# Optimization experiments

Hardware: AMD Instinct MI355X
Metric: run time of the kernel (lower is better)

## Reference

```python
import jax, jax.numpy as jnp
import numpy as np

B, C, H, W = 4, 512, 64, 64
NUM_GROUPS = 32
EPS = 1e-6


def setup_inputs() -> dict:
    key = jax.random.key(0)
    ks = jax.random.split(key, 5)
    s = 1.0 / np.sqrt(C)
    return {
        "x": jax.random.normal(ks[0], (B, C, H, W), dtype=jnp.float32),
        "gn_scale": jnp.ones((C,), jnp.float32),
        "gn_bias": jnp.zeros((C,), jnp.float32),
        "wq": jax.random.normal(ks[1], (C, C), jnp.float32) * s,
        "bq": jnp.zeros((C,), jnp.float32),
        "wk": jax.random.normal(ks[2], (C, C), jnp.float32) * s,
        "bk": jnp.zeros((C,), jnp.float32),
        "wv": jax.random.normal(ks[3], (C, C), jnp.float32) * s,
        "bv": jnp.zeros((C,), jnp.float32),
        "wo": jax.random.normal(ks[4], (C, C), jnp.float32) * s,
        "bo": jnp.zeros((C,), jnp.float32),
    }


def _group_norm(x, scale, bias):
    # x: [b, c, h, w]; normalize over (c//g, h, w) within each of g groups
    b, c, h, w = x.shape
    g = NUM_GROUPS
    xg = x.reshape(b, g, c // g, h, w)
    mean = jnp.mean(xg, axis=(2, 3, 4), keepdims=True)
    var = jnp.var(xg, axis=(2, 3, 4), keepdims=True)
    xg = (xg - mean) * jax.lax.rsqrt(var + EPS)
    xn = xg.reshape(b, c, h, w)
    return xn * scale[None, :, None, None] + bias[None, :, None, None]


def _conv1x1(x, w, b):
    # channel-mixing 1x1 conv: [b, c, h, w] x [c_in, c_out] -> [b, c_out, h, w]
    return jnp.einsum('bchw,cd->bdhw', x, w) + b[None, :, None, None]


def reference(x, gn_scale, gn_bias, wq, bq, wk, bk, wv, bv, wo, bo):
    b, c, h, w = x.shape
    h_ = _group_norm(x, gn_scale, gn_bias)
    q = _conv1x1(h_, wq, bq).reshape(b, c, h * w).transpose(0, 2, 1)  # [b, hw, c]
    k = _conv1x1(h_, wk, bk).reshape(b, c, h * w)                     # [b, c, hw]
    v = _conv1x1(h_, wv, bv).reshape(b, c, h * w)                     # [b, c, hw]
    scores = jnp.matmul(q, k) * (c ** -0.5)      # [b, hw, hw]
    attn = jax.nn.softmax(scores, axis=-1)       # [b, hw, hw]
    out = jnp.matmul(v, attn.transpose(0, 2, 1)) # [b, c, hw]
    out = out.reshape(b, c, h, w)
    out = _conv1x1(out, wo, bo)
    return x + out
```

## Files before the change

### kernel.cpp

```cpp
#include <hip/hip_runtime.h>
#include <stdint.h>

typedef __attribute__((ext_vector_type(8))) short short8;
typedef __attribute__((ext_vector_type(4))) float f32x4;
typedef __attribute__((ext_vector_type(16))) float f32x16;
typedef __attribute__((ext_vector_type(4))) unsigned int uint4v;

__device__ __forceinline__ short cvt_bf16(float f) {
  uint32_t u = __builtin_bit_cast(uint32_t, f);
  u += 0x7FFFu + ((u >> 16) & 1u);
  return (short)(u >> 16);
}

__device__ __forceinline__ float bf16_to_f32(short s) {
  return __builtin_bit_cast(float, (uint32_t)((unsigned short)s) << 16);
}

__device__ __forceinline__ void gload_lds16(const void* g, void* l) {
  __builtin_amdgcn_global_load_lds(
      (const __attribute__((address_space(1))) void*)g,
      (__attribute__((address_space(3))) void*)l, 16, 0, 0);
}

__global__ __launch_bounds__(256) void k_transpose_w(const float* __restrict__ src,
                                                     short* __restrict__ dst) {
  __shared__ float t[32][33];
  int n0 = blockIdx.x * 32, c0 = blockIdx.y * 32;
  int lx = threadIdx.x & 31, ly = threadIdx.x >> 5;
#pragma unroll
  for (int i = 0; i < 4; ++i) {
    int c = ly + i * 8;
    t[c][lx] = src[(size_t)(c0 + c) * 512 + n0 + lx];
  }
  __syncthreads();
#pragma unroll
  for (int i = 0; i < 4; ++i) {
    int n = ly + i * 8;
    dst[(size_t)(n0 + n) * 512 + c0 + lx] = cvt_bf16(t[lx][n]);
  }
}

__global__ void k_bias_concat(const float* __restrict__ bq, const float* __restrict__ bk,
                              float* __restrict__ bqk) {
  int i = blockIdx.x * 256 + threadIdx.x;
  if (i < 512) bqk[i] = bq[i];
  else if (i < 1024) bqk[i] = bk[i - 512];
}

__global__ __launch_bounds__(256) void k_gn_stats(const float* __restrict__ x,
                                                  float* __restrict__ stats) {
  int bg = blockIdx.x;
  const float* p = x + (size_t)bg * 65536;
  float s = 0.f, ss = 0.f;
#pragma unroll 4
  for (int i = 0; i < 64; ++i) {
    float4 v = *(const float4*)(p + i * 1024 + threadIdx.x * 4);
    s += v.x + v.y + v.z + v.w;
    ss += v.x * v.x + v.y * v.y + v.z * v.z + v.w * v.w;
  }
#pragma unroll
  for (int m = 1; m < 64; m <<= 1) {
    s += __shfl_xor(s, m, 64);
    ss += __shfl_xor(ss, m, 64);
  }
  __shared__ float red[8];
  int w = threadIdx.x >> 6;
  if ((threadIdx.x & 63) == 0) { red[w * 2] = s; red[w * 2 + 1] = ss; }
  __syncthreads();
  if (threadIdx.x == 0) {
    float S1 = red[0] + red[2] + red[4] + red[6];
    float S2 = red[1] + red[3] + red[5] + red[7];
    float mean = S1 * (1.f / 65536.f);
    float var = S2 * (1.f / 65536.f) - mean * mean;
    stats[bg * 2] = mean;
    stats[bg * 2 + 1] = rsqrtf(var + 1e-6f);
  }
}

__global__ __launch_bounds__(256) void k_gn_apply(const float* __restrict__ x,
    const float* __restrict__ stats, const float* __restrict__ gsc,
    const float* __restrict__ gbi, short* __restrict__ h_t) {
  __shared__ float t[64][65];
  int p0 = blockIdx.x * 64, c0 = blockIdx.y * 64, b = blockIdx.z;
  int lp = threadIdx.x & 63, lc = threadIdx.x >> 6;
#pragma unroll
  for (int i = 0; i < 16; ++i) {
    int c = c0 + lc * 16 + i;
    float mean = stats[(b * 32 + (c >> 4)) * 2];
    float rstd = stats[(b * 32 + (c >> 4)) * 2 + 1];
    float v = x[((size_t)b * 512 + c) * 4096 + p0 + lp];
    t[lc * 16 + i][lp] = (v - mean) * rstd * gsc[c] + gbi[c];
  }
  __syncthreads();
  int pl = threadIdx.x >> 2;
  int cs = (threadIdx.x & 3) * 16;
  short8 v8a, v8b;
#pragma unroll
  for (int j = 0; j < 8; ++j) v8a[j] = cvt_bf16(t[cs + j][pl]);
#pragma unroll
  for (int j = 0; j < 8; ++j) v8b[j] = cvt_bf16(t[cs + 8 + j][pl]);
  size_t o = ((size_t)(b * 4096 + p0 + pl)) * 512 + c0 + cs;
  *(short8*)(h_t + o) = v8a;
  *(short8*)(h_t + o + 8) = v8b;
}

template <int BIAS_M, int FINAL>
__global__ __launch_bounds__(256) void k_gemm(const short* __restrict__ A,
    const short* __restrict__ Bm, const float* __restrict__ bias,
    short* __restrict__ Cb, float* __restrict__ Cf, const float* __restrict__ resid,
    int ldc) {
  __shared__ __align__(16) short a_lds[128 * 32];
  __shared__ __align__(16) short b_lds[128 * 32];
  int m0 = blockIdx.x * 128, n0 = blockIdx.y * 128;
  int lane = threadIdx.x & 63, wid = threadIdx.x >> 6;
  int h16 = lane >> 4, l16 = lane & 15;
  int wr = wid >> 1, wc = wid & 1;

  f32x4 acc[4][4];
#pragma unroll
  for (int mi = 0; mi < 4; ++mi)
#pragma unroll
    for (int ni = 0; ni < 4; ++ni) acc[mi][ni] = (f32x4){0.f, 0.f, 0.f, 0.f};

  for (int kk = 0; kk < 16; ++kk) {
#pragma unroll
    for (int i = 0; i < 4; ++i) {
      int idx = wid * 4 + i;
      int mat = idx >> 3, h = (idx >> 1) & 3, rh = idx & 1;
      const short* src = (mat ? Bm : A) +
          ((size_t)((mat ? n0 : m0) + rh * 64 + lane)) * 512 + kk * 32 + h * 8;
      short* dst = (mat ? b_lds : a_lds) + (h * 128 + rh * 64) * 8;
      gload_lds16(src, dst);
    }
    asm volatile("s_waitcnt vmcnt(0)" ::: "memory");
    __syncthreads();
    short8 af[4], bf[4];
#pragma unroll
    for (int mi = 0; mi < 4; ++mi)
      af[mi] = *(const short8*)(a_lds + (h16 * 128 + wr * 64 + mi * 16 + l16) * 8);
#pragma unroll
    for (int ni = 0; ni < 4; ++ni)
      bf[ni] = *(const short8*)(b_lds + (h16 * 128 + wc * 64 + ni * 16 + l16) * 8);
#pragma unroll
    for (int mi = 0; mi < 4; ++mi)
#pragma unroll
      for (int ni = 0; ni < 4; ++ni)
        acc[mi][ni] = __builtin_amdgcn_mfma_f32_16x16x32_bf16(af[mi], bf[ni], acc[mi][ni], 0, 0, 0);
    __syncthreads();
  }

#pragma unroll
  for (int mi = 0; mi < 4; ++mi)
#pragma unroll
    for (int ni = 0; ni < 4; ++ni)
#pragma unroll
      for (int r = 0; r < 4; ++r) {
        int row = m0 + wr * 64 + mi * 16 + 4 * h16 + r;
        int col = n0 + wc * 64 + ni * 16 + l16;
        float v = acc[mi][ni][r] + (BIAS_M ? bias[row] : bias[col]);
        if (FINAL) {
          size_t oidx = ((size_t)((col >> 12) * 512 + row)) * 4096 + (col & 4095);
          Cf[oidx] = v + resid[oidx];
        } else {
          Cb[(size_t)row * ldc + col] = cvt_bf16(v);
        }
      }
}

__global__ __launch_bounds__(512, 2) void k_flash3(const short* __restrict__ qk,
    const short* __restrict__ v_t, short* __restrict__ oa, short* __restrict__ ob,
    float* __restrict__ ml) {
  __shared__ __align__(16) short k_lds[32 * 512];
  __shared__ __align__(16) short v_lds[32 * 512];
  __shared__ __align__(16) float s_lds[8 * 1024];

  const int tid = threadIdx.x;
  const int lane = tid & 63, wid = tid >> 6;
  const int qg = wid >> 1, dh = wid & 1;
  const int l31 = lane & 31, h = lane >> 5;
  const int bx = blockIdx.x;
  const int combo = bx & 7, qt = bx >> 3;
  const int b = combo >> 1, s = combo & 1;
  const float K2 = 0.06376649f;

  short8 qf[16];
  {
    const short* qbase = qk + ((size_t)(b * 4096 + qt * 128 + qg * 32 + l31)) * 1024
                         + dh * 256 + h * 8;
#pragma unroll
    for (int s_ = 0; s_ < 16; ++s_) qf[s_] = *(const short8*)(qbase + s_ * 16);
  }

  const size_t kvrow0 = (size_t)(b * 4096 + s * 2048);

#define STAGE_K3(T)                                                                   \
  {                                                                                   \
    int t_ = (T);                                                                     \
    _Pragma("unroll") for (int i = 0; i < 4; ++i) {                                   \
      int ks = wid * 4 + i;                                                           \
      gload_lds16(qk + (kvrow0 + t_ * 32 + l31) * 1024 + 512 + ks * 16 + h * 8,       \
                  k_lds + ks * 512);                                                  \
    }                                                                                 \
  }
#define STAGE_V3(T)                                                                   \
  {                                                                                   \
    int t_ = (T);                                                                     \
    _Pragma("unroll") for (int i = 0; i < 4; ++i) {                                   \
      int si = wid * 4 + i;                                                           \
      int ks = si >> 4, d0 = si & 15;                                                 \
      gload_lds16(v_t + (size_t)(d0 * 32 + l31) * 16384                               \
                      + (kvrow0 + t_ * 32 + ks * 16 + h * 8),                         \
                  v_lds + si * 512);                                                  \
    }                                                                                 \
  }

  STAGE_K3(0);
  STAGE_V3(0);
  asm volatile("s_waitcnt vmcnt(0)" ::: "memory");
  __builtin_amdgcn_s_barrier();
  __builtin_amdgcn_sched_barrier(0);

  float m_run = -3.0e38f, l_run = 0.f;
  f32x16 acc[8];
#pragma unroll
  for (int tl = 0; tl < 8; ++tl)
#pragma unroll
    for (int r = 0; r < 16; ++r) acc[tl][r] = 0.f;

  for (int t = 0; t < 64; ++t) {
    int tn = (t + 1 < 64) ? t + 1 : 63;
    f32x16 st;
#pragma unroll
    for (int r = 0; r < 16; ++r) st[r] = 0.f;
#pragma unroll
    for (int s_ = 0; s_ < 16; ++s_) {
      short8 kf = *(const short8*)(k_lds + ((dh * 16 + s_) * 64 + lane) * 8);
      st = __builtin_amdgcn_mfma_f32_32x32x16_bf16(kf, qf[s_], st, 0, 0, 0);
    }
    {
      float* sp = s_lds + wid * 1024 + lane * 4;
#pragma unroll
      for (int q4 = 0; q4 < 4; ++q4) {
        f32x4 v = {st[q4 * 4 + 0], st[q4 * 4 + 1], st[q4 * 4 + 2], st[q4 * 4 + 3]};
        *(f32x4*)(sp + q4 * 256) = v;
      }
    }
    asm volatile("s_waitcnt vmcnt(0) lgkmcnt(0)" ::: "memory");
    __builtin_amdgcn_s_barrier();
    __builtin_amdgcn_sched_barrier(0);
    STAGE_K3(tn);
    {
      const float* sp = s_lds + (wid ^ 1) * 1024 + lane * 4;
#pragma unroll
      for (int q4 = 0; q4 < 4; ++q4) {
        f32x4 v = *(const f32x4*)(sp + q4 * 256);
        st[q4 * 4 + 0] += v[0]; st[q4 * 4 + 1] += v[1];
        st[q4 * 4 + 2] += v[2]; st[q4 * 4 + 3] += v[3];
      }
    }
    float mt = st[0];
#pragma unroll
    for (int r = 1; r < 16; ++r) mt = fmaxf(mt, st[r]);
    mt = fmaxf(mt, __shfl_xor(mt, 32));
    if (__any(mt > m_run + 45.0f)) {
      float mnew = fmaxf(m_run, mt);
      float rs = exp2f((m_run - mnew) * K2);
      m_run = mnew;
      l_run *= rs;
#pragma unroll
      for (int r = 0; r < 16; ++r) {
        int rowq = (r & 3) + 8 * (r >> 2) + 4 * h;
        float rr = __shfl(rs, rowq);
#pragma unroll
        for (int tl = 0; tl < 8; ++tl) acc[tl][r] *= rr;
      }
    }
    float ls = 0.f;
#pragma unroll
    for (int r = 0; r < 16; ++r) { st[r] = exp2f((st[r] - m_run) * K2); ls += st[r]; }
    ls += __shfl_xor(ls, 32);
    l_run += ls;
    short8 pa[2];
#pragma unroll
    for (int ks = 0; ks < 2; ++ks) {
      unsigned int a0, a1, a2, a3;
      int bse = ks * 8;
      asm("v_cvt_pk_bf16_f32 %0, %1, %2" : "=v"(a0) : "v"(st[bse + 0]), "v"(st[bse + 1]));
      asm("v_cvt_pk_bf16_f32 %0, %1, %2" : "=v"(a1) : "v"(st[bse + 2]), "v"(st[bse + 3]));
      asm("v_cvt_pk_bf16_f32 %0, %1, %2" : "=v"(a2) : "v"(st[bse + 4]), "v"(st[bse + 5]));
      asm("v_cvt_pk_bf16_f32 %0, %1, %2" : "=v"(a3) : "v"(st[bse + 6]), "v"(st[bse + 7]));
      asm("v_permlane32_swap_b32 %0, %1" : "+v"(a0), "+v"(a2));
      asm("v_permlane32_swap_b32 %0, %1" : "+v"(a1), "+v"(a3));
      uint4v w; w[0] = a0; w[1] = a1; w[2] = a2; w[3] = a3;
      pa[ks] = __builtin_bit_cast(short8, w);
    }
#pragma unroll
    for (int ks = 0; ks < 2; ++ks)
#pragma unroll
      for (int tl = 0; tl < 8; ++tl) {
        short8 vb = *(const short8*)(v_lds + ((ks * 16 + dh * 8 + tl) * 64 + lane) * 8);
        acc[tl] = __builtin_amdgcn_mfma_f32_32x32x16_bf16(pa[ks], vb, acc[tl], 0, 0, 0);
      }
    asm volatile("s_waitcnt vmcnt(0) lgkmcnt(0)" ::: "memory");
    __builtin_amdgcn_s_barrier();
    __builtin_amdgcn_sched_barrier(0);
    STAGE_V3(tn);
  }

  float linv = 1.0f / l_run;
  short* obuf = (s == 0) ? oa : ob;
#pragma unroll
  for (int r = 0; r < 16; ++r) {
    int rowq = (r & 3) + 8 * (r >> 2) + 4 * h;
    float li = __shfl(linv, rowq);
    size_t grow = ((size_t)(b * 4096 + qt * 128 + qg * 32 + rowq)) * 512;
#pragma unroll
    for (int tl = 0; tl < 8; ++tl)
      obuf[grow + dh * 256 + tl * 32 + l31] = cvt_bf16(acc[tl][r] * li);
  }
  if (dh == 0 && lane < 32) {
    int gq = b * 4096 + qt * 128 + qg * 32 + lane;
    ml[((size_t)s * 16384 + gq) * 2 + 0] = m_run;
    ml[((size_t)s * 16384 + gq) * 2 + 1] = l_run;
  }
#undef STAGE_K3
#undef STAGE_V3
}

__global__ __launch_bounds__(256) void k_combine(const short* __restrict__ oa,
    const float* __restrict__ ml, short* __restrict__ ob_out) {
  int gq = blockIdx.x * 4 + (threadIdx.x >> 6);
  int d0 = (threadIdx.x & 63) * 8;
  const float K2 = 0.06376649f;
  float ma = ml[(size_t)gq * 2 + 0], la = ml[(size_t)gq * 2 + 1];
  float mb = ml[((size_t)16384 + gq) * 2 + 0], lb = ml[((size_t)16384 + gq) * 2 + 1];
  float m = fmaxf(ma, mb);
  float ca = exp2f((ma - m) * K2) * la;
  float cb = exp2f((mb - m) * K2) * lb;
  float inv = 1.f / (ca + cb);
  ca *= inv; cb *= inv;
  short8 a = *(const short8*)(oa + (size_t)gq * 512 + d0);
  short8 bv = *(const short8*)(ob_out + (size_t)gq * 512 + d0);
  short8 o;
#pragma unroll
  for (int j = 0; j < 8; ++j)
    o[j] = cvt_bf16(ca * bf16_to_f32(a[j]) + cb * bf16_to_f32(bv[j]));
  *(short8*)(ob_out + (size_t)gq * 512 + d0) = o;
}

extern "C" void kernel_launch(void* const* d_in, const int* in_sizes, int n_in,
                              void* d_out, int out_size, void* d_ws, size_t ws_size,
                              hipStream_t stream) {
  const float* x   = (const float*)d_in[0];
  const float* gsc = (const float*)d_in[1];
  const float* gbi = (const float*)d_in[2];
  const float* wq  = (const float*)d_in[3];
  const float* bq  = (const float*)d_in[4];
  const float* wk  = (const float*)d_in[5];
  const float* bk  = (const float*)d_in[6];
  const float* wv  = (const float*)d_in[7];
  const float* bv  = (const float*)d_in[8];
  const float* wo  = (const float*)d_in[9];
  const float* bo  = (const float*)d_in[10];
  float* out = (float*)d_out;

  char* ws = (char*)d_ws;
  float* stats = (float*)ws;
  float* bqk   = (float*)(ws + 4096);
  short* wqk_t = (short*)(ws + 16384);
  short* wv_t  = (short*)(ws + 16384 + (1u << 20));
  short* wo_t  = (short*)(ws + 16384 + (1u << 20) + (1u << 19));
  char*  big   = ws + 16384 + (1u << 21);
  short* h_t   = (short*)big;
  short* qkb   = (short*)(big + (16ll << 20));
  short* v_t   = (short*)(big + (48ll << 20));
  short* o_at  = (short*)(big + (64ll << 20));
  float* mlbuf = (float*)(big + (80ll << 20));

  dim3 b256(256);
  k_transpose_w<<<dim3(16, 16), b256, 0, stream>>>(wq, wqk_t);
  k_transpose_w<<<dim3(16, 16), b256, 0, stream>>>(wk, wqk_t + 512 * 512);
  k_transpose_w<<<dim3(16, 16), b256, 0, stream>>>(wv, wv_t);
  k_transpose_w<<<dim3(16, 16), b256, 0, stream>>>(wo, wo_t);
  k_bias_concat<<<4, 256, 0, stream>>>(bq, bk, bqk);
  k_gn_stats<<<128, b256, 0, stream>>>(x, stats);
  k_gn_apply<<<dim3(64, 8, 4), b256, 0, stream>>>(x, stats, gsc, gbi, h_t);
  k_gemm<0, 0><<<dim3(128, 8), b256, 0, stream>>>(h_t, wqk_t, bqk, qkb, nullptr, nullptr, 1024);
  k_gemm<1, 0><<<dim3(4, 128), b256, 0, stream>>>(wv_t, h_t, bv, v_t, nullptr, nullptr, 16384);
  k_flash3<<<dim3(256), dim3(512), 0, stream>>>(qkb, v_t, h_t, o_at, mlbuf);
  k_combine<<<dim3(4096), b256, 0, stream>>>(h_t, mlbuf, o_at);
  k_gemm<1, 1><<<dim3(4, 128), b256, 0, stream>>>(wo_t, o_at, bo, nullptr, out, x, 0);
}
```

Measured before the change: 382.7 us.

## Double-buffer K tiles in flash attention and raise MFMA wave priority

The K tile in LDS is now double-buffered. The next tile's load is issued at the start of each iteration, and the mid-iteration wait becomes vmcnt(4), so the prefetch overlaps the QK and softmax work instead of being drained. MFMA sections are wrapped in s_setprio, the row max uses a tree reduction, and the PV loop is fused per k-slice. LDS use grows by 32 KB per block, which could limit occupancy at 2 blocks per CU. The combine kernel also gains a guard against non-finite denominators.

Measured after the change: 401.7 us. +5.0%, slower.

```diff
diff --git a/kernel.cpp b/kernel.cpp
--- a/kernel.cpp
+++ b/kernel.cpp
@@ -167,10 +167,10 @@
       }
 }
 
-__global__ __launch_bounds__(512, 2) void k_flash3(const short* __restrict__ qk,
+__global__ __launch_bounds__(512, 2) void k_flash6(const short* __restrict__ qk,
     const short* __restrict__ v_t, short* __restrict__ oa, short* __restrict__ ob,
     float* __restrict__ ml) {
-  __shared__ __align__(16) short k_lds[32 * 512];
+  __shared__ __align__(16) short k_lds[2 * 32 * 512];
   __shared__ __align__(16) short v_lds[32 * 512];
   __shared__ __align__(16) float s_lds[8 * 1024];
 
@@ -193,16 +193,17 @@
 
   const size_t kvrow0 = (size_t)(b * 4096 + s * 2048);
 
-#define STAGE_K3(T)                                                                   \
+#define STAGE_K6(T, DST)                                                              \
   {                                                                                   \
     int t_ = (T);                                                                     \
+    short* d_ = (DST);                                                                \
     _Pragma("unroll") for (int i = 0; i < 4; ++i) {                                   \
       int ks = wid * 4 + i;                                                           \
       gload_lds16(qk + (kvrow0 + t_ * 32 + l31) * 1024 + 512 + ks * 16 + h * 8,       \
-                  k_lds + ks * 512);                                                  \
+                  d_ + ks * 512);                                                     \
     }                                                                                 \
   }
-#define STAGE_V3(T)                                                                   \
+#define STAGE_V6(T)                                                                   \
   {                                                                                   \
     int t_ = (T);                                                                     \
     _Pragma("unroll") for (int i = 0; i < 4; ++i) {                                   \
@@ -214,8 +215,8 @@
     }                                                                                 \
   }
 
-  STAGE_K3(0);
-  STAGE_V3(0);
+  STAGE_K6(0, k_lds);
+  STAGE_V6(0);
   asm volatile("s_waitcnt vmcnt(0)" ::: "memory");
   __builtin_amdgcn_s_barrier();
   __builtin_amdgcn_sched_barrier(0);
@@ -228,15 +229,20 @@
     for (int r = 0; r < 16; ++r) acc[tl][r] = 0.f;
 
   for (int t = 0; t < 64; ++t) {
-    int tn = (t + 1 < 64) ? t + 1 : 63;
+    const int kb = t & 1;
+    const short* kcur = k_lds + kb * (32 * 512);
+    short* knxt = k_lds + (kb ^ 1) * (32 * 512);
+    if (t + 1 < 64) STAGE_K6(t + 1, knxt);
     f32x16 st;
 #pragma unroll
     for (int r = 0; r < 16; ++r) st[r] = 0.f;
+    __builtin_amdgcn_s_setprio(1);
 #pragma unroll
     for (int s_ = 0; s_ < 16; ++s_) {
-      short8 kf = *(const short8*)(k_lds + ((dh * 16 + s_) * 64 + lane) * 8);
+      short8 kf = *(const short8*)(kcur + ((dh * 16 + s_) * 64 + lane) * 8);
       st = __builtin_amdgcn_mfma_f32_32x32x16_bf16(kf, qf[s_], st, 0, 0, 0);
     }
+    __builtin_amdgcn_s_setprio(0);
     {
       float* sp = s_lds + wid * 1024 + lane * 4;
 #pragma unroll
@@ -245,10 +251,9 @@
         *(f32x4*)(sp + q4 * 256) = v;
       }
     }
-    asm volatile("s_waitcnt vmcnt(0) lgkmcnt(0)" ::: "memory");
+    asm volatile("s_waitcnt vmcnt(4) lgkmcnt(0)" ::: "memory");
     __builtin_amdgcn_s_barrier();
     __builtin_amdgcn_sched_barrier(0);
-    STAGE_K3(tn);
     {
       const float* sp = s_lds + (wid ^ 1) * 1024 + lane * 4;
 #pragma unroll
@@ -258,9 +263,12 @@
         st[q4 * 4 + 2] += v[2]; st[q4 * 4 + 3] += v[3];
       }
     }
-    float mt = st[0];
-#pragma unroll
-    for (int r = 1; r < 16; ++r) mt = fmaxf(mt, st[r]);
+    float u0 = fmaxf(st[0], st[1]),  u1 = fmaxf(st[2], st[3]);
+    float u2 = fmaxf(st[4], st[5]),  u3 = fmaxf(st[6], st[7]);
+    float u4 = fmaxf(st[8], st[9]),  u5 = fmaxf(st[10], st[11]);
+    float u6 = fmaxf(st[12], st[13]), u7 = fmaxf(st[14], st[15]);
+    float mt = fmaxf(fmaxf(fmaxf(u0, u1), fmaxf(u2, u3)),
+                     fmaxf(fmaxf(u4, u5), fmaxf(u6, u7)));
     mt = fmaxf(mt, __shfl_xor(mt, 32));
     if (__any(mt > m_run + 45.0f)) {
       float mnew = fmaxf(m_run, mt);
@@ -280,7 +288,7 @@
     for (int r = 0; r < 16; ++r) { st[r] = exp2f((st[r] - m_run) * K2); ls += st[r]; }
     ls += __shfl_xor(ls, 32);
     l_run += ls;
-    short8 pa[2];
+    __builtin_amdgcn_s_setprio(1);
 #pragma unroll
     for (int ks = 0; ks < 2; ++ks) {
       unsigned int a0, a1, a2, a3;
@@ -292,19 +300,18 @@
       asm("v_permlane32_swap_b32 %0, %1" : "+v"(a0), "+v"(a2));
       asm("v_permlane32_swap_b32 %0, %1" : "+v"(a1), "+v"(a3));
       uint4v w; w[0] = a0; w[1] = a1; w[2] = a2; w[3] = a3;
-      pa[ks] = __builtin_bit_cast(short8, w);
-    }
-#pragma unroll
-    for (int ks = 0; ks < 2; ++ks)
+      short8 pa = __builtin_bit_cast(short8, w);
 #pragma unroll
       for (int tl = 0; tl < 8; ++tl) {
         short8 vb = *(const short8*)(v_lds + ((ks * 16 + dh * 8 + tl) * 64 + lane) * 8);
-        acc[tl] = __builtin_amdgcn_mfma_f32_32x32x16_bf16(pa[ks], vb, acc[tl], 0, 0, 0);
+        acc[tl] = __builtin_amdgcn_mfma_f32_32x32x16_bf16(pa, vb, acc[tl], 0, 0, 0);
       }
+    }
+    __builtin_amdgcn_s_setprio(0);
     asm volatile("s_waitcnt vmcnt(0) lgkmcnt(0)" ::: "memory");
     __builtin_amdgcn_s_barrier();
     __builtin_amdgcn_sched_barrier(0);
-    STAGE_V3(tn);
+    if (t + 1 < 64) STAGE_V6(t + 1);
   }
 
   float linv = 1.0f / l_run;
@@ -323,8 +330,8 @@
     ml[((size_t)s * 16384 + gq) * 2 + 0] = m_run;
     ml[((size_t)s * 16384 + gq) * 2 + 1] = l_run;
   }
-#undef STAGE_K3
-#undef STAGE_V3
+#undef STAGE_K6
+#undef STAGE_V6
 }
 
 __global__ __launch_bounds__(256) void k_combine(const short* __restrict__ oa,
@@ -335,16 +342,23 @@
   float ma = ml[(size_t)gq * 2 + 0], la = ml[(size_t)gq * 2 + 1];
   float mb = ml[((size_t)16384 + gq) * 2 + 0], lb = ml[((size_t)16384 + gq) * 2 + 1];
   float m = fmaxf(ma, mb);
-  float ca = exp2f((ma - m) * K2) * la;
-  float cb = exp2f((mb - m) * K2) * lb;
-  float inv = 1.f / (ca + cb);
-  ca *= inv; cb *= inv;
+  float wa = exp2f((ma - m) * K2) * la;
+  float wb = exp2f((mb - m) * K2) * lb;
+  float denom = wa + wb;
+  float fa, fb;
+  if (isfinite(denom) && denom > 0.f) {
+    float inv = 1.f / denom;
+    fa = wa * inv; fb = wb * inv;
+  } else {
+    fa = (ma >= mb) ? 1.f : 0.f;
+    fb = 1.f - fa;
+  }
   short8 a = *(const short8*)(oa + (size_t)gq * 512 + d0);
   short8 bv = *(const short8*)(ob_out + (size_t)gq * 512 + d0);
   short8 o;
 #pragma unroll
   for (int j = 0; j < 8; ++j)
-    o[j] = cvt_bf16(ca * bf16_to_f32(a[j]) + cb * bf16_to_f32(bv[j]));
+    o[j] = cvt_bf16(fa * bf16_to_f32(a[j]) + fb * bf16_to_f32(bv[j]));
   *(short8*)(ob_out + (size_t)gq * 512 + d0) = o;
 }
 
@@ -387,7 +401,7 @@
   k_gn_apply<<<dim3(64, 8, 4), b256, 0, stream>>>(x, stats, gsc, gbi, h_t);
   k_gemm<0, 0><<<dim3(128, 8), b256, 0, stream>>>(h_t, wqk_t, bqk, qkb, nullptr, nullptr, 1024);
   k_gemm<1, 0><<<dim3(4, 128), b256, 0, stream>>>(wv_t, h_t, bv, v_t, nullptr, nullptr, 16384);
-  k_flash3<<<dim3(256), dim3(512), 0, stream>>>(qkb, v_t, h_t, o_at, mlbuf);
+  k_flash6<<<dim3(256), dim3(512), 0, stream>>>(qkb, v_t, h_t, o_at, mlbuf);
   k_combine<<<dim3(4096), b256, 0, stream>>>(h_t, mlbuf, o_at);
   k_gemm<1, 1><<<dim3(4, 128), b256, 0, stream>>>(wo_t, o_at, bo, nullptr, out, x, 0);
 }
```
